# Kernel optimization log

Hardware: AMD Instinct MI355X
Metric: run time of the kernel (lower is better)

The kernel has to match this reference:

```python
import jax, jax.numpy as jnp
import numpy as np

BATCH = 16384
MODEL_DIM = 768
SAE_HIDDEN = 16384
K = 3


def setup_inputs() -> dict:
    key = jax.random.key(0)
    k1, k2, k3, k4, k5 = jax.random.split(key, 5)
    scale_enc = 1.0 / np.sqrt(MODEL_DIM)
    scale_dec = 1.0 / np.sqrt(SAE_HIDDEN)
    return {
        "model_activations": jax.random.normal(k1, (BATCH, MODEL_DIM), jnp.float32),
        "W_enc": jax.random.normal(k2, (SAE_HIDDEN, MODEL_DIM), jnp.float32) * scale_enc,
        "b_enc": jax.random.normal(k3, (SAE_HIDDEN,), jnp.float32) * scale_enc,
        "W_dec": jax.random.normal(k4, (MODEL_DIM, SAE_HIDDEN), jnp.float32) * scale_dec,
        "b_dec": jax.random.normal(k5, (MODEL_DIM,), jnp.float32) * scale_dec,
    }


def reference(model_activations, W_enc, b_enc, W_dec, b_dec):
    # encoder linear: [B, D] @ [D, H] + [H] -> [B, H]
    pre_activations = model_activations @ W_enc.T + b_enc
    # top-k (k=3) per row
    topk_vals, topk_idx = jax.lax.top_k(pre_activations, K)  # [B, K]
    # scatter the k values into a zero tensor (sparse activation)
    B = pre_activations.shape[0]
    rows = jnp.arange(B)[:, None]  # [B, 1]
    sae_activations = jnp.zeros_like(pre_activations).at[rows, topk_idx].set(topk_vals)
    # number of unique live latents across the whole batch (static-shape version of torch.unique)
    live_mask = jnp.zeros((pre_activations.shape[1],), dtype=jnp.bool_).at[topk_idx.reshape(-1)].set(True)
    num_live_latents = jnp.sum(live_mask.astype(jnp.int32))
    # decoder linear: [B, H] @ [H, D] + [D] -> [B, D]
    reconstructed = sae_activations @ W_dec.T + b_dec
    return reconstructed, num_live_latents
```

## Files before the change

### kernel.cpp

```cpp
#include <hip/hip_runtime.h>
#include <cstdint>
#include <cstddef>

#define B_ROWS 16384
#define DIM    768
#define HID    16384
#define BM     256
#define BK     64
#define KT_N   (DIM / BK)
#define NCB    (HID / BM)

typedef __bf16 bf16x8 __attribute__((ext_vector_type(8)));
typedef float  f32x4  __attribute__((ext_vector_type(4)));
typedef unsigned int   u32;
typedef unsigned short u16;

__device__ __forceinline__ u32 umaxu(u32 a, u32 b) { return a > b ? a : b; }
__device__ __forceinline__ u32 uminu(u32 a, u32 b) { return a < b ? a : b; }

__device__ __forceinline__ u16 f2bf(float f) {
    u32 u = __float_as_uint(f);
    return (u16)((u + 0x7FFFu + ((u >> 16) & 1u)) >> 16);
}

__device__ __forceinline__ u32 pk(float v, int gidx) {
    u32 b = __float_as_uint(v);
    u32 t = b >> 16;
    t ^= (b & 0x80000000u) ? 0xFFFFu : 0x8000u;
    return (t << 16) | (u32)gidx;
}

__device__ __forceinline__ void gll16(const void* g, void* l) {
    __builtin_amdgcn_global_load_lds(
        (const __attribute__((address_space(1))) unsigned int*)g,
        (__attribute__((address_space(3))) unsigned int*)l, 16, 0, 0);
}

__device__ __forceinline__ void merge3(u32& z0, u32& z1, u32& z2,
                                       u32 A0, u32 A1, u32 A2,
                                       u32 B0, u32 B1, u32 B2) {
    const u32 P = uminu(A0, B0), Q = umaxu(A1, B1);
    const u32 R = uminu(A1, B1), S = umaxu(A2, B2);
    z0 = umaxu(A0, B0);
    z1 = umaxu(P, Q);
    z2 = umaxu(umaxu(uminu(P, Q), R), S);
}

__device__ __forceinline__ bool better(float v1, int i1, float v2, int i2) {
    return (v1 > v2) || (v1 == v2 && i1 < i2);
}
__device__ __forceinline__ void ins3(float v, int i,
                                     float& v0, int& i0, float& v1, int& i1,
                                     float& v2, int& i2) {
    if (better(v, i, v2, i2)) {
        v2 = v; i2 = i;
        if (better(v2, i2, v1, i1)) { float tv = v1; int ti = i1; v1 = v2; i1 = i2; v2 = tv; i2 = ti; }
        if (better(v1, i1, v0, i0)) { float tv = v0; int ti = i0; v0 = v1; i0 = i1; v1 = tv; i1 = ti; }
    }
}

__global__ __launch_bounds__(256) void cast_bf16(const float* __restrict__ X,
                                                 const float* __restrict__ W,
                                                 u16* __restrict__ Xb, u16* __restrict__ Wb) {
    const int n4 = (B_ROWS * DIM) / 4;
    for (int i = blockIdx.x * blockDim.x + threadIdx.x; i < n4; i += gridDim.x * blockDim.x) {
        float4 x = ((const float4*)X)[i];
        float4 w = ((const float4*)W)[i];
        ushort4 xo, wo;
        xo.x = f2bf(x.x); xo.y = f2bf(x.y); xo.z = f2bf(x.z); xo.w = f2bf(x.w);
        wo.x = f2bf(w.x); wo.y = f2bf(w.y); wo.z = f2bf(w.z); wo.w = f2bf(w.w);
        ((ushort4*)Xb)[i] = xo;
        ((ushort4*)Wb)[i] = wo;
    }
}

__global__ __launch_bounds__(512, 2) void gemm_screen(const u16* __restrict__ Xb,
                                                      const u16* __restrict__ Wb,
                                                      const float* __restrict__ benc,
                                                      u32* __restrict__ pvpi) {
    __shared__ __align__(16) u16 As[2 * BM * BK];
    __shared__ __align__(16) u16 Bs[2 * BM * BK];

    const int bid = blockIdx.x;
    const int wg = ((bid & 7) << 9) | (bid >> 3);
    const int st = wg >> 8, loc = wg & 255;
    const int rb = ((st >> 2) << 4) | (loc >> 4);
    const int cb = ((st & 3) << 4) | (loc & 15);
    const int rowBase = rb * BM, colBase = cb * BM;

    const int tid = threadIdx.x;
    const int wid = tid >> 6, lane = tid & 63;
    const int wm = wid >> 2, wn = wid & 3;
    const int j = lane & 15, g = lane >> 4;
    const int js = j & 7;

    const int sr = tid >> 3, ss = tid & 7;
    const int sc = ss ^ (sr & 7);
    const u32 aoff = (u32)(rowBase + sr) * DIM + (u32)sc * 8;
    const u32 boff = (u32)(colBase + sr) * DIM + (u32)sc * 8;
    const int lbw = wid * 512;

#define STAGE_A(H, KTL, D1) do { \
    gll16(Xb + aoff + (H) * 98304u + (u32)(KTL) * 64u,           As + (D1) * 16384 + (H) * 8192 + lbw); \
    gll16(Xb + aoff + (H) * 98304u + 49152u + (u32)(KTL) * 64u,  As + (D1) * 16384 + (H) * 8192 + 4096 + lbw); \
} while (0)
#define STAGE_B(H, KTL, D1) do { \
    gll16(Wb + boff + (H) * 98304u + (u32)(KTL) * 64u,           Bs + (D1) * 16384 + (H) * 8192 + lbw); \
    gll16(Wb + boff + (H) * 98304u + 49152u + (u32)(KTL) * 64u,  Bs + (D1) * 16384 + (H) * 8192 + 4096 + lbw); \
} while (0)

    const bf16x8* As8 = (const bf16x8*)As;
    const bf16x8* Bs8 = (const bf16x8*)Bs;

#define READ_A(MH, D) do { \
    _Pragma("unroll") for (int mtl = 0; mtl < 4; ++mtl) { \
        const int m8_ = (D) * 2048 + (wm * 128 + ((MH) * 4 + mtl) * 16 + j) * 8; \
        aF[mtl][0] = As8[m8_ + ((0 + g) ^ js)]; \
        aF[mtl][1] = As8[m8_ + ((4 + g) ^ js)]; \
    } } while (0)
#define READ_B(DST, NH, D) do { \
    _Pragma("unroll") for (int ntl = 0; ntl < 2; ++ntl) { \
        const int n8_ = (D) * 2048 + (wn * 64 + ((NH) * 2 + ntl) * 16 + j) * 8; \
        DST[ntl][0] = Bs8[n8_ + ((0 + g) ^ js)]; \
        DST[ntl][1] = Bs8[n8_ + ((4 + g) ^ js)]; \
    } } while (0)

#define MFMA_Q(MH, NH, BF) do { \
    __builtin_amdgcn_s_setprio(1); \
    _Pragma("unroll") for (int kk2 = 0; kk2 < 2; ++kk2) \
    _Pragma("unroll") for (int mtl = 0; mtl < 4; ++mtl) \
    _Pragma("unroll") for (int ntl = 0; ntl < 2; ++ntl) \
        acc[(MH) * 4 + mtl][(NH) * 2 + ntl] = __builtin_amdgcn_mfma_f32_16x16x32_bf16( \
            aF[mtl][kk2], BF[ntl][kk2], acc[(MH) * 4 + mtl][(NH) * 2 + ntl], 0, 0, 0); \
    __builtin_amdgcn_s_setprio(0); \
} while (0)

    f32x4 acc[8][4];
#pragma unroll
    for (int mt = 0; mt < 8; ++mt)
#pragma unroll
        for (int nt = 0; nt < 4; ++nt) acc[mt][nt] = (f32x4){0.f, 0.f, 0.f, 0.f};

    STAGE_A(0, 0, 0); STAGE_B(0, 0, 0); STAGE_B(1, 0, 0); STAGE_A(1, 0, 0);
    asm volatile("s_waitcnt vmcnt(4)" ::: "memory");
    __builtin_amdgcn_s_barrier();

    bf16x8 aF[4][2], bLo[2][2], bHi[2][2];

#pragma unroll 1
    for (int t = 0; t < KT_N; ++t) {
        const int d = t & 1, d1 = d ^ 1;
        const bool stg = (t + 1 < KT_N);
        const int kt = t + 1;

        READ_A(0, d);
        READ_B(bLo, 0, d);
        if (stg) STAGE_A(0, kt, d1);
        __builtin_amdgcn_s_barrier();
        MFMA_Q(0, 0, bLo);
        if (stg) asm volatile("s_waitcnt vmcnt(4)" ::: "memory");
        else     asm volatile("s_waitcnt vmcnt(2)" ::: "memory");
        __builtin_amdgcn_s_barrier();

        READ_B(bHi, 1, d);
        if (stg) STAGE_B(0, kt, d1);
        __builtin_amdgcn_s_barrier();
        MFMA_Q(0, 1, bHi);
        if (stg) asm volatile("s_waitcnt vmcnt(4)" ::: "memory");
        else     asm volatile("s_waitcnt vmcnt(0)" ::: "memory");
        __builtin_amdgcn_s_barrier();

        READ_A(1, d);
        if (stg) STAGE_B(1, kt, d1);
        __builtin_amdgcn_s_barrier();
        MFMA_Q(1, 1, bHi);
        __builtin_amdgcn_s_barrier();

        if (stg) STAGE_A(1, kt, d1);
        __builtin_amdgcn_s_barrier();
        MFMA_Q(1, 0, bLo);
        if (stg) asm volatile("s_waitcnt vmcnt(4)" ::: "memory");
        __builtin_amdgcn_s_barrier();
    }

    __syncthreads();
    u32* sm = (u32*)As;

    float bias[4]; int gcol[4];
#pragma unroll
    for (int nt = 0; nt < 4; ++nt) {
        gcol[nt] = colBase + wn * 64 + nt * 16 + j;
        bias[nt] = benc[gcol[nt]];
    }

#pragma unroll
    for (int mt = 0; mt < 8; ++mt) {
#pragma unroll
        for (int reg = 0; reg < 4; ++reg) {
            const u32 k0 = pk(acc[mt][0][reg] + bias[0], gcol[0]);
            const u32 k1 = pk(acc[mt][1][reg] + bias[1], gcol[1]);
            const u32 k2 = pk(acc[mt][2][reg] + bias[2], gcol[2]);
            const u32 k3 = pk(acc[mt][3][reg] + bias[3], gcol[3]);
            u32 a0 = umaxu(k0, k1), a1 = uminu(k0, k1);
            u32 b0 = umaxu(k2, k3), b1 = uminu(k2, k3);
            u32 x0 = umaxu(a0, b0);
            u32 p = uminu(a0, b0), q = umaxu(a1, b1), r2 = uminu(a1, b1);
            u32 x1 = umaxu(p, q);
            u32 x2 = umaxu(uminu(p, q), r2);
#pragma unroll
            for (int mk = 1; mk < 16; mk <<= 1) {
                const u32 y0 = (u32)__shfl_xor((int)x0, mk, 64);
                const u32 y1 = (u32)__shfl_xor((int)x1, mk, 64);
                const u32 y2 = (u32)__shfl_xor((int)x2, mk, 64);
                u32 z0, z1, z2;
                merge3(z0, z1, z2, x0, x1, x2, y0, y1, y2);
                x0 = z0; x1 = z1; x2 = z2;
            }
            if ((lane & 15) == 0) {
                const int row = wm * 128 + mt * 16 + g * 4 + reg;
                sm[row * 12 + wn * 3 + 0] = x0;
                sm[row * 12 + wn * 3 + 1] = x1;
                sm[row * 12 + wn * 3 + 2] = x2;
            }
        }
    }
    __syncthreads();
    if (tid < 256) {
        const int row = tid;
        const u32* s = sm + row * 12;
        u32 m0, m1, m2, n0, n1, n2, z0, z1, z2;
        merge3(m0, m1, m2, s[0], s[1], s[2], s[3], s[4], s[5]);
        merge3(n0, n1, n2, s[6], s[7], s[8], s[9], s[10], s[11]);
        merge3(z0, z1, z2, m0, m1, m2, n0, n1, n2);
        const size_t base = ((size_t)(rowBase + row) * NCB + cb) * 3;
        pvpi[base + 0] = z0; pvpi[base + 1] = z1; pvpi[base + 2] = z2;
    }
#undef STAGE_A
#undef STAGE_B
#undef READ_A
#undef READ_B
#undef MFMA_Q
}

__global__ __launch_bounds__(256) void reduce_recheck(
        const u32* __restrict__ pvpi, const float* __restrict__ X,
        const float* __restrict__ Wenc, const float* __restrict__ benc,
        float* __restrict__ fv, int* __restrict__ fi, int* __restrict__ mask) {
    const int wid = threadIdx.x >> 6, lane = threadIdx.x & 63;
    const int row = blockIdx.x * 4 + wid;

    const u32* p = pvpi + (size_t)row * (NCB * 3);
    u32 k[3];
#pragma unroll
    for (int t = 0; t < 3; t++) k[t] = p[t * 64 + lane];

    u32 cand[16];
#pragma unroll
    for (int it = 0; it < 16; ++it) {
        u32 m = umaxu(umaxu(k[0], k[1]), k[2]);
#pragma unroll
        for (int mk = 1; mk < 64; mk <<= 1) m = umaxu(m, (u32)__shfl_xor((int)m, mk, 64));
        cand[it] = m;
#pragma unroll
        for (int t = 0; t < 3; t++) if (k[t] == m) k[t] = 0;
    }

    const float4* xp = (const float4*)(X + (size_t)row * DIM) + lane * 3;
    const float4 x0 = xp[0], x1 = xp[1], x2 = xp[2];

    float v0 = -INFINITY, v1 = -INFINITY, v2 = -INFINITY;
    int   i0 = 0x7fffffff, i1 = 0x7fffffff, i2 = 0x7fffffff;
#pragma unroll
    for (int it = 0; it < 16; ++it) {
        const int ci = (int)(cand[it] & 0xFFFFu);
        const float4* wq = (const float4*)(Wenc + (size_t)ci * DIM) + lane * 3;
        const float4 w0 = wq[0], w1 = wq[1], w2 = wq[2];
        float s = x0.x * w0.x;
        s = fmaf(x0.y, w0.y, s); s = fmaf(x0.z, w0.z, s); s = fmaf(x0.w, w0.w, s);
        s = fmaf(x1.x, w1.x, s); s = fmaf(x1.y, w1.y, s); s = fmaf(x1.z, w1.z, s);
        s = fmaf(x1.w, w1.w, s); s = fmaf(x2.x, w2.x, s); s = fmaf(x2.y, w2.y, s);
        s = fmaf(x2.z, w2.z, s); s = fmaf(x2.w, w2.w, s);
#pragma unroll
        for (int mk = 1; mk < 64; mk <<= 1) s += __shfl_xor(s, mk, 64);
        const float val = s + benc[ci];
        ins3(val, ci, v0, i0, v1, i1, v2, i2);
    }
    if (lane == 0) {
        fv[row * 3 + 0] = v0; fv[row * 3 + 1] = v1; fv[row * 3 + 2] = v2;
        fi[row * 3 + 0] = i0; fi[row * 3 + 1] = i1; fi[row * 3 + 2] = i2;
        mask[i0] = 1; mask[i1] = 1; mask[i2] = 1;
    }
}

__global__ __launch_bounds__(256) void count_live(const int* __restrict__ mask,
                                                  float* __restrict__ outScalar) {
    __shared__ int sd[256];
    const int tid = threadIdx.x;
    int s = 0;
    for (int i = tid; i < HID; i += 256) s += mask[i];
    sd[tid] = s;
    __syncthreads();
    for (int st = 128; st > 0; st >>= 1) {
        if (tid < st) sd[tid] += sd[tid + st];
        __syncthreads();
    }
    if (tid == 0) outScalar[0] = (float)sd[0];
}

__global__ __launch_bounds__(256) void transpose_wdec(const float* __restrict__ W,
                                                      float* __restrict__ Wt) {
    __shared__ float t[32][33];
    const int bx = blockIdx.x;
    const int by = blockIdx.y;
    const int x = threadIdx.x & 31;
    const int y = threadIdx.x >> 5;
#pragma unroll
    for (int i = 0; i < 4; i++) {
        const int d = by * 32 + y + i * 8;
        t[y + i * 8][x] = W[(size_t)d * HID + bx * 32 + x];
    }
    __syncthreads();
#pragma unroll
    for (int i = 0; i < 4; i++) {
        const int h = bx * 32 + y + i * 8;
        Wt[(size_t)h * DIM + by * 32 + x] = t[x][y + i * 8];
    }
}

__global__ __launch_bounds__(192) void decode_rows(
        const float* __restrict__ fv, const int* __restrict__ fi,
        const float* __restrict__ Wt, const float* __restrict__ bdec,
        float* __restrict__ out) {
    const int row = blockIdx.x;
    const int tid = threadIdx.x;
    const float v0 = fv[row * 3 + 0], v1 = fv[row * 3 + 1], v2 = fv[row * 3 + 2];
    const int   i0 = fi[row * 3 + 0], i1 = fi[row * 3 + 1], i2 = fi[row * 3 + 2];
    const int jj = tid * 4;
    const float4 b  = *(const float4*)(bdec + jj);
    const float4 w0 = *(const float4*)(Wt + (size_t)i0 * DIM + jj);
    const float4 w1 = *(const float4*)(Wt + (size_t)i1 * DIM + jj);
    const float4 w2 = *(const float4*)(Wt + (size_t)i2 * DIM + jj);
    float4 o;
    o.x = b.x + v0 * w0.x + v1 * w1.x + v2 * w2.x;
    o.y = b.y + v0 * w0.y + v1 * w1.y + v2 * w2.y;
    o.z = b.z + v0 * w0.z + v1 * w1.z + v2 * w2.z;
    o.w = b.w + v0 * w0.w + v1 * w1.w + v2 * w2.w;
    *(float4*)(out + (size_t)row * DIM + jj) = o;
}

extern "C" void kernel_launch(void* const* d_in, const int* in_sizes, int n_in,
                              void* d_out, int out_size, void* d_ws, size_t ws_size,
                              hipStream_t stream) {
    const float* X    = (const float*)d_in[0];
    const float* Wenc = (const float*)d_in[1];
    const float* benc = (const float*)d_in[2];
    const float* Wdec = (const float*)d_in[3];
    const float* bdec = (const float*)d_in[4];
    float* out = (float*)d_out;

    char* ws = (char*)d_ws;
    u16*   Xb   = (u16*)ws;
    u16*   Wb   = (u16*)(ws + 25165824);
    float* Wt   = (float*)ws;
    u32*   pvpi = (u32*)(ws + 50331648);
    float* fv   = (float*)(ws + 62914560);
    int*   fi   = (int*)(ws + 63111168);
    int*   mask = (int*)(ws + 63307776);

    hipMemsetAsync(mask, 0, HID * sizeof(int), stream);

    cast_bf16<<<3072, 256, 0, stream>>>(X, Wenc, Xb, Wb);
    gemm_screen<<<4096, 512, 0, stream>>>(Xb, Wb, benc, pvpi);
    reduce_recheck<<<B_ROWS / 4, 256, 0, stream>>>(pvpi, X, Wenc, benc, fv, fi, mask);
    count_live<<<1, 256, 0, stream>>>(mask, out + (size_t)B_ROWS * DIM);
    transpose_wdec<<<dim3(HID / 32, DIM / 32), 256, 0, stream>>>(Wdec, Wt);
    decode_rows<<<B_ROWS, 192, 0, stream>>>(fv, fi, Wt, bdec, out);
}
```

Baseline: 858.3 us.

## Swap MFMA operands for row-per-lane epilogue and restructure staging pipeline

The A and B operands of the MFMA are swapped, so each lane's accumulator registers now hold consecutive columns of a single row. The top-3 epilogue then does an in-register insertion over 16 values per lane, needs only two cross-lane shuffle stages instead of four, and loads the bias with float4 reads. In the main loop, global-to-LDS staging is issued earlier (A0 and B0 together at the start), the vmcnt waits are loosened, and two barriers per iteration are dropped. This reduces shuffle and synchronisation overhead but makes the LDS double-buffer hazards and the wait counts more delicate.

```diff
diff --git a/kernel.cpp b/kernel.cpp
--- a/kernel.cpp
+++ b/kernel.cpp
@@ -131,7 +131,7 @@
     _Pragma("unroll") for (int mtl = 0; mtl < 4; ++mtl) \
     _Pragma("unroll") for (int ntl = 0; ntl < 2; ++ntl) \
         acc[(MH) * 4 + mtl][(NH) * 2 + ntl] = __builtin_amdgcn_mfma_f32_16x16x32_bf16( \
-            aF[mtl][kk2], BF[ntl][kk2], acc[(MH) * 4 + mtl][(NH) * 2 + ntl], 0, 0, 0); \
+            BF[ntl][kk2], aF[mtl][kk2], acc[(MH) * 4 + mtl][(NH) * 2 + ntl], 0, 0, 0); \
     __builtin_amdgcn_s_setprio(0); \
 } while (0)
 
@@ -153,31 +153,27 @@
         const bool stg = (t + 1 < KT_N);
         const int kt = t + 1;
 
+        if (stg) { STAGE_A(0, kt, d1); STAGE_B(0, kt, d1); }
         READ_A(0, d);
         READ_B(bLo, 0, d);
-        if (stg) STAGE_A(0, kt, d1);
         __builtin_amdgcn_s_barrier();
         MFMA_Q(0, 0, bLo);
-        if (stg) asm volatile("s_waitcnt vmcnt(4)" ::: "memory");
+        if (stg) asm volatile("s_waitcnt vmcnt(6)" ::: "memory");
         else     asm volatile("s_waitcnt vmcnt(2)" ::: "memory");
         __builtin_amdgcn_s_barrier();
 
+        if (stg) STAGE_B(1, kt, d1);
         READ_B(bHi, 1, d);
-        if (stg) STAGE_B(0, kt, d1);
         __builtin_amdgcn_s_barrier();
         MFMA_Q(0, 1, bHi);
-        if (stg) asm volatile("s_waitcnt vmcnt(4)" ::: "memory");
+        if (stg) asm volatile("s_waitcnt vmcnt(6)" ::: "memory");
         else     asm volatile("s_waitcnt vmcnt(0)" ::: "memory");
         __builtin_amdgcn_s_barrier();
 
+        if (stg) STAGE_A(1, kt, d1);
         READ_A(1, d);
-        if (stg) STAGE_B(1, kt, d1);
         __builtin_amdgcn_s_barrier();
         MFMA_Q(1, 1, bHi);
-        __builtin_amdgcn_s_barrier();
-
-        if (stg) STAGE_A(1, kt, d1);
-        __builtin_amdgcn_s_barrier();
         MFMA_Q(1, 0, bLo);
         if (stg) asm volatile("s_waitcnt vmcnt(4)" ::: "memory");
         __builtin_amdgcn_s_barrier();
@@ -186,42 +182,40 @@
     __syncthreads();
     u32* sm = (u32*)As;
 
-    float bias[4]; int gcol[4];
+    float bias[4][4];
 #pragma unroll
     for (int nt = 0; nt < 4; ++nt) {
-        gcol[nt] = colBase + wn * 64 + nt * 16 + j;
-        bias[nt] = benc[gcol[nt]];
-    }
+        const float4 b4 = *(const float4*)(benc + colBase + wn * 64 + nt * 16 + g * 4);
+        bias[nt][0] = b4.x; bias[nt][1] = b4.y; bias[nt][2] = b4.z; bias[nt][3] = b4.w;
+    }
+    const int cb0 = colBase + wn * 64 + g * 4;
 
 #pragma unroll
     for (int mt = 0; mt < 8; ++mt) {
-#pragma unroll
-        for (int reg = 0; reg < 4; ++reg) {
-            const u32 k0 = pk(acc[mt][0][reg] + bias[0], gcol[0]);
-            const u32 k1 = pk(acc[mt][1][reg] + bias[1], gcol[1]);
-            const u32 k2 = pk(acc[mt][2][reg] + bias[2], gcol[2]);
-            const u32 k3 = pk(acc[mt][3][reg] + bias[3], gcol[3]);
-            u32 a0 = umaxu(k0, k1), a1 = uminu(k0, k1);
-            u32 b0 = umaxu(k2, k3), b1 = uminu(k2, k3);
-            u32 x0 = umaxu(a0, b0);
-            u32 p = uminu(a0, b0), q = umaxu(a1, b1), r2 = uminu(a1, b1);
-            u32 x1 = umaxu(p, q);
-            u32 x2 = umaxu(uminu(p, q), r2);
-#pragma unroll
-            for (int mk = 1; mk < 16; mk <<= 1) {
-                const u32 y0 = (u32)__shfl_xor((int)x0, mk, 64);
-                const u32 y1 = (u32)__shfl_xor((int)x1, mk, 64);
-                const u32 y2 = (u32)__shfl_xor((int)x2, mk, 64);
-                u32 z0, z1, z2;
-                merge3(z0, z1, z2, x0, x1, x2, y0, y1, y2);
-                x0 = z0; x1 = z1; x2 = z2;
+        u32 x0 = 0, x1 = 0, x2 = 0;
+#pragma unroll
+        for (int nt = 0; nt < 4; ++nt) {
+#pragma unroll
+            for (int reg = 0; reg < 4; ++reg) {
+                const u32 k = pk(acc[mt][nt][reg] + bias[nt][reg], cb0 + nt * 16 + reg);
+                const u32 t1 = uminu(x0, k), t2 = uminu(x1, k);
+                x0 = umaxu(x0, k); x1 = umaxu(x1, t1); x2 = umaxu(x2, t2);
             }
-            if ((lane & 15) == 0) {
-                const int row = wm * 128 + mt * 16 + g * 4 + reg;
-                sm[row * 12 + wn * 3 + 0] = x0;
-                sm[row * 12 + wn * 3 + 1] = x1;
-                sm[row * 12 + wn * 3 + 2] = x2;
-            }
+        }
+#pragma unroll
+        for (int mk = 16; mk <= 32; mk <<= 1) {
+            const u32 y0 = (u32)__shfl_xor((int)x0, mk, 64);
+            const u32 y1 = (u32)__shfl_xor((int)x1, mk, 64);
+            const u32 y2 = (u32)__shfl_xor((int)x2, mk, 64);
+            u32 z0, z1, z2;
+            merge3(z0, z1, z2, x0, x1, x2, y0, y1, y2);
+            x0 = z0; x1 = z1; x2 = z2;
+        }
+        if (lane < 16) {
+            const int row = wm * 128 + mt * 16 + j;
+            sm[row * 12 + wn * 3 + 0] = x0;
+            sm[row * 12 + wn * 3 + 1] = x1;
+            sm[row * 12 + wn * 3 + 2] = x2;
         }
     }
     __syncthreads();
```

After: 973.5 us. 1.13x slower.
